# Optimization experiments

Hardware: AMD Instinct MI355X
Metric: run time of the kernel (lower is better)

Reference implementation:

```python
import jax, jax.numpy as jnp
import numpy as np

C_IN = 336      # input feature channels
Z = 6           # height bins per BEV cell (2016 = Z * C_IN)
BEV_H, BEV_W = 240, 120
L = Z * BEV_H * BEV_W  # 172800 voxels
HF, WF = 160, 256      # fisheye feature map size


def setup_inputs() -> dict:
    key = jax.random.key(0)
    k1, k2, k3, k4, k5 = jax.random.split(key, 5)
    inp = jax.random.normal(k1, (1, C_IN, HF, WF), dtype=jnp.float32)
    uu = jax.random.randint(k2, (L,), 0, WF, dtype=jnp.int32)
    vv = jax.random.randint(k3, (L,), 0, HF, dtype=jnp.int32)
    valid = jax.random.uniform(k4, (L,), dtype=jnp.float32)
    density = jax.random.uniform(k5, (L,), dtype=jnp.float32)
    return {"input": inp, "uu": uu, "vv": vv, "valid": valid, "density": density}


def reference(input, uu, vv, valid, density):
    # Gather per-voxel pixel features, weight by valid*density, lay out as BEV grid.
    B, C, Hf, Wf = input.shape
    idx = vv * Wf + uu                         # [L] flat pixel index per voxel
    flat = input.reshape(B, C, Hf * Wf)        # [B, C, Hf*Wf]
    gathered = jnp.take(flat, idx, axis=2)     # [B, C, L]
    w = valid * density                        # [L]
    weighted = gathered * w                    # [B, C, L]
    # voxel ordering: L = Z * BEV_H * BEV_W
    out = weighted.reshape(B, C, Z, BEV_H, BEV_W)
    out = out.transpose(0, 2, 1, 3, 4).reshape(B, Z * C, BEV_H, BEV_W)  # [1, 2016, 240, 120]
    return out
```

## Files before the change

### kernel.cpp

```cpp
#include <hip/hip_runtime.h>
#include <hip/hip_fp16.h>


#define C_IN  336
#define ZB    6
#define BEV_H 240
#define BEV_W 120
#define LVOX  (ZB * BEV_H * BEV_W)
#define HF    160
#define WF    256
#define PIX   (HF * WF)
#define HW    (BEV_H * BEV_W)

#define ROWH  384
#define CHH   128

typedef float f32x4 __attribute__((ext_vector_type(4)));

#define TA_P 64
#define TA_C 48
__global__ __launch_bounds__(256) void transpose_f16_kernel(
    const float* __restrict__ in, __half* __restrict__ T2)
{
    __shared__ float tile[TA_C][TA_P + 1];
    const int p0 = blockIdx.x * TA_P;
    const int c0 = blockIdx.y * TA_C;
    const int t  = threadIdx.x;

    #pragma unroll
    for (int i = 0; i < (TA_P * TA_C) / 256; ++i) {
        int idx = i * 256 + t;
        int cl = idx >> 6;
        int pl = idx & 63;
        tile[cl][pl] = in[(size_t)(c0 + cl) * PIX + p0 + pl];
    }
    __syncthreads();
    #pragma unroll
    for (int i = 0; i < (TA_P * TA_C / 2) / 256; ++i) {
        int idx = i * 256 + t;
        int cl2 = idx % (TA_C / 2);
        int pl  = idx / (TA_C / 2);
        int c   = c0 + 2 * cl2;
        int chunk = c / 112;
        int poff  = chunk * CHH + (c - chunk * 112);
        __half2 hv = __floats2half2_rn(tile[2 * cl2][pl], tile[2 * cl2 + 1][pl]);
        *reinterpret_cast<__half2*>(&T2[(size_t)(p0 + pl) * ROWH + poff]) = hv;
    }
}

#define VB   64
#define CC   112
#define NCH  (C_IN / CC)
#define LROW (VB + 1)
#define NGPV (CC / 4)
#define NG   ((VB * NGPV) / 256)

__global__ __launch_bounds__(256) void gather_f16_kernel(
    const __half* __restrict__ T2,
    const int*    __restrict__ uu,
    const int*    __restrict__ vv,
    const float*  __restrict__ valid,
    const float*  __restrict__ density,
    float*        __restrict__ out)
{
    __shared__ float tile[CC * LROW];
    __shared__ int   p_s[VB];
    __shared__ float w_s[VB];

    const int t   = threadIdx.x;
    const int l0  = blockIdx.x * VB;
    const int z   = l0 / HW;
    const int hw0 = l0 - z * HW;

    if (t < VB) {
        int l = l0 + t;
        p_s[t] = vv[l] * WF + uu[l];
        w_s[t] = valid[l] * density[l];
    }
    __syncthreads();

    int   vi[NG], gi[NG], myp[NG];
    float myw[NG];
    #pragma unroll
    for (int i = 0; i < NG; ++i) {
        int idx = i * 256 + t;
        vi[i]  = idx / NGPV;
        gi[i]  = idx - vi[i] * NGPV;
        myp[i] = p_s[vi[i]];
        myw[i] = w_s[vi[i]];
    }

    uint2 pf[NG];
    #pragma unroll
    for (int i = 0; i < NG; ++i)
        pf[i] = *reinterpret_cast<const uint2*>(
            &T2[(size_t)myp[i] * ROWH + gi[i] * 4]);

    #pragma unroll
    for (int ch = 0; ch < NCH; ++ch) {
        #pragma unroll
        for (int i = 0; i < NG; ++i) {
            const float2 f01 = __half22float2(*reinterpret_cast<const __half2*>(&pf[i].x));
            const float2 f23 = __half22float2(*reinterpret_cast<const __half2*>(&pf[i].y));
            const float w = myw[i];
            int base = (gi[i] * 4) * LROW + vi[i];
            tile[base]          = f01.x * w;
            tile[base + LROW]   = f01.y * w;
            tile[base + 2*LROW] = f23.x * w;
            tile[base + 3*LROW] = f23.y * w;
        }
        __syncthreads();

        if (ch + 1 < NCH) {
            #pragma unroll
            for (int i = 0; i < NG; ++i)
                pf[i] = *reinterpret_cast<const uint2*>(
                    &T2[(size_t)myp[i] * ROWH + (ch + 1) * CHH + gi[i] * 4]);
        }

        {
            const int vq = (t & 15) * 4;
            const int cb = t >> 4;
            #pragma unroll
            for (int i2 = 0; i2 < CC / 16; ++i2) {
                int cl = i2 * 16 + cb;
                f32x4 o;
                o.x = tile[cl * LROW + vq + 0];
                o.y = tile[cl * LROW + vq + 1];
                o.z = tile[cl * LROW + vq + 2];
                o.w = tile[cl * LROW + vq + 3];
                __builtin_nontemporal_store(o, reinterpret_cast<f32x4*>(
                    &out[(size_t)(z * C_IN + ch * CC + cl) * HW + hw0 + vq]));
            }
        }
        __syncthreads();
    }
}

#define CPT 16
__global__ __launch_bounds__(256) void voxel_proj_direct(
    const float* __restrict__ input,
    const int*   __restrict__ uu,
    const int*   __restrict__ vv,
    const float* __restrict__ valid,
    const float* __restrict__ density,
    float*       __restrict__ out)
{
    const int l = blockIdx.x * 256 + threadIdx.x;
    const int p = vv[l] * WF + uu[l];
    const float w = valid[l] * density[l];
    const int z  = l / HW;
    const int hw = l - z * HW;
    const float* inb  = input + p;
    float*       outb = out + (size_t)z * C_IN * HW + hw;
    const int c0 = blockIdx.y * CPT;
    #pragma unroll
    for (int i = 0; i < CPT; ++i) {
        const int c = c0 + i;
        outb[(size_t)c * HW] = inb[(size_t)c * PIX] * w;
    }
}

extern "C" void kernel_launch(void* const* d_in, const int* in_sizes, int n_in,
                              void* d_out, int out_size, void* d_ws, size_t ws_size,
                              hipStream_t stream)
{
    const float* input   = (const float*)d_in[0];
    const int*   uu      = (const int*)  d_in[1];
    const int*   vv      = (const int*)  d_in[2];
    const float* valid   = (const float*)d_in[3];
    const float* density = (const float*)d_in[4];
    float*       out     = (float*)d_out;

    const size_t T_bytes = (size_t)PIX * ROWH * sizeof(__half);
    if (ws_size >= T_bytes) {
        __half* T2 = (__half*)d_ws;
        transpose_f16_kernel<<<dim3(PIX / TA_P, C_IN / TA_C), dim3(256), 0, stream>>>(input, T2);
        gather_f16_kernel<<<dim3(LVOX / VB), dim3(256), 0, stream>>>(T2, uu, vv, valid, density, out);
    } else {
        voxel_proj_direct<<<dim3(LVOX / 256, C_IN / CPT), dim3(256), 0, stream>>>(
            input, uu, vv, valid, density, out);
    }
}
```

Measured before the change: 72.52 us.

## Pack fp16 transposed rows densely and gather with 16-byte loads

Shrinks the intermediate fp16 pixel-major buffer from a padded 384-half row (three 128-slot chunks) to a dense 336-half row, which cuts transpose write and gather read bytes. The gather now fetches 8 halves per thread with uint4 loads instead of 4 halves with uint2 loads, with 3.5 groups per thread, so the last group is predicated on half the threads. The transpose's input reads become nontemporal loads. A 336-half row is 672 bytes, so 16-byte loads stay aligned, but rows no longer start on cache-line boundaries and the uneven per-thread work adds divergence.

```diff
diff --git a/kernel.cpp b/kernel.cpp
--- a/kernel.cpp
+++ b/kernel.cpp
@@ -11,9 +11,7 @@
 #define WF    256
 #define PIX   (HF * WF)
 #define HW    (BEV_H * BEV_W)
-
-#define ROWH  384
-#define CHH   128
+#define ROWH  336
 
 typedef float f32x4 __attribute__((ext_vector_type(4)));
 
@@ -32,7 +30,8 @@
         int idx = i * 256 + t;
         int cl = idx >> 6;
         int pl = idx & 63;
-        tile[cl][pl] = in[(size_t)(c0 + cl) * PIX + p0 + pl];
+        tile[cl][pl] = __builtin_nontemporal_load(
+            &in[(size_t)(c0 + cl) * PIX + p0 + pl]);
     }
     __syncthreads();
     #pragma unroll
@@ -40,11 +39,9 @@
         int idx = i * 256 + t;
         int cl2 = idx % (TA_C / 2);
         int pl  = idx / (TA_C / 2);
-        int c   = c0 + 2 * cl2;
-        int chunk = c / 112;
-        int poff  = chunk * CHH + (c - chunk * 112);
         __half2 hv = __floats2half2_rn(tile[2 * cl2][pl], tile[2 * cl2 + 1][pl]);
-        *reinterpret_cast<__half2*>(&T2[(size_t)(p0 + pl) * ROWH + poff]) = hv;
+        *reinterpret_cast<__half2*>(
+            &T2[(size_t)(p0 + pl) * ROWH + c0 + 2 * cl2]) = hv;
     }
 }
 
@@ -52,8 +49,8 @@
 #define CC   112
 #define NCH  (C_IN / CC)
 #define LROW (VB + 1)
-#define NGPV (CC / 4)
-#define NG   ((VB * NGPV) / 256)
+#define GPV  (CC / 8)
+#define GPC  (VB * GPV)
 
 __global__ __launch_bounds__(256) void gather_f16_kernel(
     const __half* __restrict__ T2,
@@ -79,43 +76,56 @@
     }
     __syncthreads();
 
-    int   vi[NG], gi[NG], myp[NG];
-    float myw[NG];
+    int   qg[4];
+    float qw[4];
+    const __half* qbase[4];
     #pragma unroll
-    for (int i = 0; i < NG; ++i) {
-        int idx = i * 256 + t;
-        vi[i]  = idx / NGPV;
-        gi[i]  = idx - vi[i] * NGPV;
-        myp[i] = p_s[vi[i]];
-        myw[i] = w_s[vi[i]];
+    for (int i = 0; i < 4; ++i) {
+        if (i < 3 || t < 128) {
+            int q = i * 256 + t;
+            int v = q / GPV;
+            qg[i] = q - v * GPV;
+            qw[i] = w_s[v];
+            qbase[i] = T2 + (size_t)p_s[v] * ROWH + qg[i] * 8;
+        }
     }
 
-    uint2 pf[NG];
+    uint4 pf[4];
     #pragma unroll
-    for (int i = 0; i < NG; ++i)
-        pf[i] = *reinterpret_cast<const uint2*>(
-            &T2[(size_t)myp[i] * ROWH + gi[i] * 4]);
+    for (int i = 0; i < 4; ++i)
+        if (i < 3 || t < 128)
+            pf[i] = *reinterpret_cast<const uint4*>(qbase[i]);
 
     #pragma unroll
     for (int ch = 0; ch < NCH; ++ch) {
         #pragma unroll
-        for (int i = 0; i < NG; ++i) {
-            const float2 f01 = __half22float2(*reinterpret_cast<const __half2*>(&pf[i].x));
-            const float2 f23 = __half22float2(*reinterpret_cast<const __half2*>(&pf[i].y));
-            const float w = myw[i];
-            int base = (gi[i] * 4) * LROW + vi[i];
-            tile[base]          = f01.x * w;
-            tile[base + LROW]   = f01.y * w;
-            tile[base + 2*LROW] = f23.x * w;
-            tile[base + 3*LROW] = f23.y * w;
+        for (int i = 0; i < 4; ++i) {
+            if (i < 3 || t < 128) {
+                int q = i * 256 + t;
+                int v = q / GPV;
+                const float2 f0 = __half22float2(*reinterpret_cast<const __half2*>(&pf[i].x));
+                const float2 f1 = __half22float2(*reinterpret_cast<const __half2*>(&pf[i].y));
+                const float2 f2 = __half22float2(*reinterpret_cast<const __half2*>(&pf[i].z));
+                const float2 f3 = __half22float2(*reinterpret_cast<const __half2*>(&pf[i].w));
+                const float w = qw[i];
+                int base = (qg[i] * 8) * LROW + v;
+                tile[base]          = f0.x * w;
+                tile[base + LROW]   = f0.y * w;
+                tile[base + 2*LROW] = f1.x * w;
+                tile[base + 3*LROW] = f1.y * w;
+                tile[base + 4*LROW] = f2.x * w;
+                tile[base + 5*LROW] = f2.y * w;
+                tile[base + 6*LROW] = f3.x * w;
+                tile[base + 7*LROW] = f3.y * w;
+            }
         }
         __syncthreads();
 
         if (ch + 1 < NCH) {
             #pragma unroll
-            for (int i = 0; i < NG; ++i)
-                pf[i] = *reinterpret_cast<const uint2*>(
-                    &T2[(size_t)myp[i] * ROWH + (ch + 1) * CHH + gi[i] * 4]);
+            for (int i = 0; i < 4; ++i)
+                if (i < 3 || t < 128)
+                    pf[i] = *reinterpret_cast<const uint4*>(qbase[i] + (ch + 1) * CC);
         }
 
         {
```

Result: slower. 75.69 us (+4.4%).
